# Performance work log

Measured on AMD Instinct MI355X. Metric: run time of the kernel, lower is better.

## Reference

```python
import jax, jax.numpy as jnp
import numpy as np
import math

HID = 128
NH = 8
HD = HID // NH
NL = 3
CLIP = 10.0
EPS = 1e-5

def _ln(x, g, b):
    mu = jnp.mean(x, axis=-1, keepdims=True)
    var = jnp.var(x, axis=-1, keepdims=True)
    return (x - mu) * jax.lax.rsqrt(var + EPS) * g + b

def _layer(h, e_bias1, e_gate2, g1, b1, wh, g2, b2, w1, w2):
    B, N, _ = h.shape
    h_in = h
    hn = _ln(h, g1, b1)
    qkv = hn @ wh                                   # (B,N,3H)
    q, k, v = jnp.split(qkv, 3, axis=-1)
    q = q.reshape(B, N, NH, HD).transpose(0, 2, 1, 3)  # (B,nh,N,hd)
    k = k.reshape(B, N, NH, HD).transpose(0, 2, 1, 3)
    v = v.reshape(B, N, NH, HD).transpose(0, 2, 1, 3)
    att = jnp.einsum('bhid,bhjd->bhij', q, k) * (1.0 / math.sqrt(HD))
    att = jax.nn.softmax(att + e_bias1, axis=-1) * e_gate2
    y = jnp.einsum('bhij,bhjd->bhid', att, v)
    y = y.transpose(0, 2, 1, 3).reshape(B, N, HID)
    z = _ln(y + h_in, g2, b2)
    mlp = jax.nn.relu(z @ w1) @ w2
    return mlp + y

def setup_inputs() -> dict:
    key = jax.random.key(0)
    ks = jax.random.split(key, 9)
    d = {
        'node_features': jax.random.normal(ks[0], (16, 256, 2), jnp.float32),
        'edge_features': jax.random.normal(ks[1], (16, 256, 256, 1), jnp.float32),
        'Wn': jax.random.normal(ks[2], (2, HID), jnp.float32) * 0.5,
        'We_in': jax.random.normal(ks[3], (1, HID), jnp.float32) * 0.1,
        'ln1_g': jnp.ones((NL, HID), jnp.float32),
        'ln1_b': jnp.zeros((NL, HID), jnp.float32),
        'Wh': jax.random.normal(ks[4], (NL, HID, 3 * HID), jnp.float32) * (1.0 / math.sqrt(HID)),
        'We': jax.random.normal(ks[5], (NL, HID, 2 * NH), jnp.float32) * (1.0 / math.sqrt(HID)),
        'ln2_g': jnp.ones((NL, HID), jnp.float32),
        'ln2_b': jnp.zeros((NL, HID), jnp.float32),
        'W1': jax.random.normal(ks[6], (NL, HID, 4 * HID), jnp.float32) * (1.0 / math.sqrt(HID)),
        'W2': jax.random.normal(ks[7], (NL, 4 * HID, HID), jnp.float32) * (1.0 / math.sqrt(4 * HID)),
        'Wdec': jax.random.normal(ks[8], (HID, 1), jnp.float32) * (1.0 / math.sqrt(HID)),
    }
    return d

def reference(node_features, edge_features, Wn, We_in, ln1_g, ln1_b, Wh, We, ln2_g, ln2_b, W1, W2, Wdec):
    h = node_features @ Wn                              # (B,N,H)
    e = edge_features @ We_in                           # (B,N,N,H)
    for i in range(NL):
        ee = e @ We[i]                                  # (B,N,N,2*nh)
        ee = ee.transpose(0, 3, 1, 2)                   # (B,2*nh,N,N)
        e1, e2 = ee[:, :NH], ee[:, NH:]
        h = _layer(h, e1, e2, ln1_g[i], ln1_b[i], Wh[i], ln2_g[i], ln2_b[i], W1[i], W2[i])
    out = h @ Wdec                                      # (B,N,1)
    out = CLIP * jnp.tanh(out / math.sqrt(HID))
    return out
```

## Files before the change

### kernel.cpp

```cpp
#include <hip/hip_runtime.h>
#include <math.h>

#define HID 128
#define NHEAD 8
#define NL 3
#define NS 256
#define ROWS 4096

typedef __attribute__((ext_vector_type(8))) short bf16x8;
typedef __attribute__((ext_vector_type(4))) float f32x4;

__device__ __forceinline__ float us2f(unsigned short s) { return __uint_as_float(((unsigned)s) << 16); }
__device__ __forceinline__ unsigned short f2b(float f) {
    unsigned u = __float_as_uint(f);
    return (unsigned short)((u + 0x7fff + ((u >> 16) & 1)) >> 16);
}

__global__ __launch_bounds__(256) void k_prep(
    const float* __restrict__ Wh, const float* __restrict__ W1, const float* __restrict__ W2,
    const float* __restrict__ We_in, const float* __restrict__ We,
    const float* __restrict__ nf, const float* __restrict__ Wn,
    unsigned short* __restrict__ WhH, unsigned short* __restrict__ WhL,
    unsigned short* __restrict__ W1H, unsigned short* __restrict__ W1L,
    unsigned short* __restrict__ W2H, unsigned short* __restrict__ W2L,
    float* __restrict__ sbuf, float* __restrict__ h)
{
    int b = blockIdx.x, t = threadIdx.x;
    if (b >= 529) {
        int idx = (b - 529) * 256 + t;
        int r = idx >> 7, c = idx & 127;
        h[idx] = nf[2 * r] * Wn[c] + nf[2 * r + 1] * Wn[HID + c];
        return;
    }
    if (b == 528) {
        if (t < NL * 2 * NHEAD) {
            int l = t / (2 * NHEAD), j = t % (2 * NHEAD);
            float acc = 0.f;
            for (int c = 0; c < HID; ++c)
                acc += We_in[c] * We[(long)(l * HID + c) * (2 * NHEAD) + j];
            sbuf[t] = acc;
        }
        return;
    }
    const float* S; unsigned short *OH, *OL; int K, N, kt, nt;
    if (b < 144) {
        int l = b / 48, rem = b % 48; kt = rem & 3; nt = rem >> 2; K = 128; N = 384;
        S = Wh + (long)l * 128 * 384; OH = WhH + (long)l * 384 * 128; OL = WhL + (long)l * 384 * 128;
    } else if (b < 336) {
        int b2 = b - 144; int l = b2 / 64, rem = b2 % 64; kt = rem & 3; nt = rem >> 2; K = 128; N = 512;
        S = W1 + (long)l * 128 * 512; OH = W1H + (long)l * 512 * 128; OL = W1L + (long)l * 512 * 128;
    } else {
        int b2 = b - 336; int l = b2 / 64, rem = b2 % 64; kt = rem & 15; nt = rem >> 4; K = 512; N = 128;
        S = W2 + (long)l * 512 * 128; OH = W2H + (long)l * 128 * 512; OL = W2L + (long)l * 128 * 512;
    }
    __shared__ float sm[32][33];
    int i0 = t >> 5, j = t & 31;
#pragma unroll
    for (int p = 0; p < 4; ++p) {
        int i = i0 + p * 8;
        sm[i][j] = S[(long)(kt * 32 + i) * N + nt * 32 + j];
    }
    __syncthreads();
#pragma unroll
    for (int p = 0; p < 4; ++p) {
        int n = i0 + p * 8;
        float v = sm[j][n];
        unsigned short hh = f2b(v);
        long o = (long)(nt * 32 + n) * K + kt * 32 + j;
        OH[o] = hh; OL[o] = f2b(v - us2f(hh));
    }
}

__global__ __launch_bounds__(256) void k_fgemm(
    const float* __restrict__ x, const float* __restrict__ x2,
    const float* __restrict__ g, const float* __restrict__ b,
    const unsigned short* __restrict__ WH, const unsigned short* __restrict__ WL,
    unsigned short* __restrict__ Ch, unsigned short* __restrict__ Cl,
    int Nc, int mode)
{
    __shared__ unsigned short sAh[64 * 136], sAl[64 * 136];
    __shared__ unsigned short sWh[64 * 136], sWl[64 * 136];
    int t = threadIdx.x;
    int row0 = blockIdx.y * 64, col0 = blockIdx.x * 64;

#pragma unroll
    for (int p = 0; p < 4; ++p) {
        int rr = (t >> 4) + p * 16, ck = t & 15;
        *(uint4*)&sWh[rr * 136 + ck * 8] = *(const uint4*)&WH[(long)(col0 + rr) * 128 + ck * 8];
        *(uint4*)&sWl[rr * 136 + ck * 8] = *(const uint4*)&WL[(long)(col0 + rr) * 128 + ck * 8];
    }
#pragma unroll
    for (int pass = 0; pass < 2; ++pass) {
        int row = pass * 32 + (t >> 3);
        int p = t & 7, cb = p * 16;
        float v[16];
        const float* xp = x + (long)(row0 + row) * HID + cb;
#pragma unroll
        for (int j = 0; j < 16; j += 4) *(float4*)&v[j] = *(const float4*)(xp + j);
        if (x2) {
            const float* yp = x2 + (long)(row0 + row) * HID + cb;
#pragma unroll
            for (int j = 0; j < 16; j += 4) {
                float4 r4 = *(const float4*)(yp + j);
                v[j] += r4.x; v[j+1] += r4.y; v[j+2] += r4.z; v[j+3] += r4.w;
            }
        }
        float s = 0.f, s2 = 0.f;
#pragma unroll
        for (int j = 0; j < 16; ++j) { s += v[j]; s2 += v[j] * v[j]; }
        s  += __shfl_xor(s, 1);  s  += __shfl_xor(s, 2);  s  += __shfl_xor(s, 4);
        s2 += __shfl_xor(s2, 1); s2 += __shfl_xor(s2, 2); s2 += __shfl_xor(s2, 4);
        float mu  = s * (1.f / HID);
        float var = s2 * (1.f / HID) - mu * mu;
        float inv = rsqrtf(var + 1e-5f);
        unsigned short hi[16], lo[16];
#pragma unroll
        for (int j = 0; j < 16; ++j) {
            int c = cb + j;
            float o = (v[j] - mu) * inv * g[c] + b[c];
            hi[j] = f2b(o); lo[j] = f2b(o - us2f(hi[j]));
        }
        *(uint4*)&sAh[row * 136 + cb]     = *(uint4*)&hi[0];
        *(uint4*)&sAh[row * 136 + cb + 8] = *(uint4*)&hi[8];
        *(uint4*)&sAl[row * 136 + cb]     = *(uint4*)&lo[0];
        *(uint4*)&sAl[row * 136 + cb + 8] = *(uint4*)&lo[8];
    }
    __syncthreads();

    int w = t >> 6, lane = t & 63;
    int m = lane & 15, quad = lane >> 4;
    f32x4 acc[4];
#pragma unroll
    for (int i = 0; i < 4; ++i) acc[i] = (f32x4){0.f, 0.f, 0.f, 0.f};
#pragma unroll
    for (int c = 0; c < 4; ++c) {
        bf16x8 ah = *(const bf16x8*)&sAh[(w * 16 + m) * 136 + c * 32 + quad * 8];
        bf16x8 al = *(const bf16x8*)&sAl[(w * 16 + m) * 136 + c * 32 + quad * 8];
#pragma unroll
        for (int nt = 0; nt < 4; ++nt) {
            bf16x8 wh = *(const bf16x8*)&sWh[(nt * 16 + m) * 136 + c * 32 + quad * 8];
            bf16x8 wl = *(const bf16x8*)&sWl[(nt * 16 + m) * 136 + c * 32 + quad * 8];
            acc[nt] = __builtin_amdgcn_mfma_f32_16x16x32_bf16(ah, wh, acc[nt], 0, 0, 0);
            acc[nt] = __builtin_amdgcn_mfma_f32_16x16x32_bf16(ah, wl, acc[nt], 0, 0, 0);
            acc[nt] = __builtin_amdgcn_mfma_f32_16x16x32_bf16(al, wh, acc[nt], 0, 0, 0);
        }
    }
#pragma unroll
    for (int nt = 0; nt < 4; ++nt) {
#pragma unroll
        for (int r = 0; r < 4; ++r) {
            int row = row0 + w * 16 + quad * 4 + r;
            int col = col0 + nt * 16 + m;
            float v = acc[nt][r];
            if (mode) v = fmaxf(v, 0.f);
            unsigned short hh = f2b(v);
            Ch[(long)row * Nc + col] = hh;
            Cl[(long)row * Nc + col] = f2b(v - us2f(hh));
        }
    }
}

__global__ __launch_bounds__(256, 3) void k_w2ln(
    const unsigned short* __restrict__ Ah, const unsigned short* __restrict__ Al,
    const unsigned short* __restrict__ WH, const unsigned short* __restrict__ WL,
    const float* __restrict__ yres, float* __restrict__ hout,
    const float* __restrict__ Wdec, float* __restrict__ out)
{
    __shared__ unsigned short sA[2][16 * 72];
    __shared__ unsigned short sW[2][128 * 72];
    int t = threadIdx.x;
    int row0 = blockIdx.x * 16;
    int w = t >> 6, lane = t & 63;
    int m = lane & 15, quad = lane >> 4;
    f32x4 acc[2];
    acc[0] = (f32x4){0.f,0.f,0.f,0.f}; acc[1] = (f32x4){0.f,0.f,0.f,0.f};

    for (int ks = 0; ks < 512; ks += 64) {
        if (ks) __syncthreads();
        {
            int pl = t >> 7, tt = t & 127;
            int r = tt >> 3, ck = tt & 7;
            const unsigned short* src = pl ? Al : Ah;
            *(uint4*)&sA[pl][r * 72 + ck * 8] = *(const uint4*)&src[(long)(row0 + r) * 512 + ks + ck * 8];
        }
        {
            int r0 = t >> 3, ck = t & 7;
#pragma unroll
            for (int p = 0; p < 4; ++p) {
                int n = r0 + p * 32;
                *(uint4*)&sW[0][n * 72 + ck * 8] = *(const uint4*)&WH[(long)n * 512 + ks + ck * 8];
                *(uint4*)&sW[1][n * 72 + ck * 8] = *(const uint4*)&WL[(long)n * 512 + ks + ck * 8];
            }
        }
        __syncthreads();
#pragma unroll
        for (int c = 0; c < 2; ++c) {
            bf16x8 ah = *(const bf16x8*)&sA[0][m * 72 + c * 32 + quad * 8];
            bf16x8 al = *(const bf16x8*)&sA[1][m * 72 + c * 32 + quad * 8];
#pragma unroll
            for (int nt = 0; nt < 2; ++nt) {
                int n = w * 32 + nt * 16 + m;
                bf16x8 wh = *(const bf16x8*)&sW[0][n * 72 + c * 32 + quad * 8];
                bf16x8 wl = *(const bf16x8*)&sW[1][n * 72 + c * 32 + quad * 8];
                acc[nt] = __builtin_amdgcn_mfma_f32_16x16x32_bf16(ah, wh, acc[nt], 0, 0, 0);
                acc[nt] = __builtin_amdgcn_mfma_f32_16x16x32_bf16(ah, wl, acc[nt], 0, 0, 0);
                acc[nt] = __builtin_amdgcn_mfma_f32_16x16x32_bf16(al, wh, acc[nt], 0, 0, 0);
            }
        }
    }
    __syncthreads();
    float* ht = (float*)&sW[0][0];
#pragma unroll
    for (int nt = 0; nt < 2; ++nt) {
#pragma unroll
        for (int r = 0; r < 4; ++r) {
            int row = quad * 4 + r;
            int col = w * 32 + nt * 16 + m;
            float v = acc[nt][r] + yres[(long)(row0 + row) * HID + col];
            hout[(long)(row0 + row) * HID + col] = v;
            ht[row * 132 + col] = v;
        }
    }
    __syncthreads();
    if (Wdec) {
        int row = t >> 4, sub = t & 15;
        float v[8];
        *(float4*)&v[0] = *(const float4*)&ht[row * 132 + sub * 8];
        *(float4*)&v[4] = *(const float4*)&ht[row * 132 + sub * 8 + 4];
        float a = 0.f;
#pragma unroll
        for (int j = 0; j < 8; ++j) a += v[j] * Wdec[sub * 8 + j];
        a += __shfl_xor(a, 1); a += __shfl_xor(a, 2); a += __shfl_xor(a, 4); a += __shfl_xor(a, 8);
        if (sub == 0) out[row0 + row] = 10.f * tanhf(a * 0.08838834764831845f);
    }
}

#define PAS 268
#define KQS 20
__global__ __launch_bounds__(256) void k_attn(
    const unsigned short* __restrict__ qkvH, const unsigned short* __restrict__ qkvL,
    const float* __restrict__ ef, const float* __restrict__ sbuf,
    int layer, float* __restrict__ y)
{
    __shared__ unsigned short Kh[NS * KQS], Kl[NS * KQS];
    __shared__ unsigned short Qh[64 * KQS], Ql[64 * KQS];
    __shared__ unsigned short Vh[16 * PAS], Vl[16 * PAS];
    __shared__ unsigned short Pa[4][16 * PAS];
    int bid = blockIdx.x;
    int q4 = bid & 3, hh = (bid >> 2) & 7, bb = bid >> 5;
    int t = threadIdx.x;
    {
        long kb = ((long)(bb * NS + t)) * 384 + HID + hh * 16;
        union { uint4 u[2]; unsigned short s[16]; } KH, KL, VH, VL;
        KH.u[0] = *(const uint4*)&qkvH[kb];       KH.u[1] = *(const uint4*)&qkvH[kb + 8];
        KL.u[0] = *(const uint4*)&qkvL[kb];       KL.u[1] = *(const uint4*)&qkvL[kb + 8];
        VH.u[0] = *(const uint4*)&qkvH[kb + 128]; VH.u[1] = *(const uint4*)&qkvH[kb + 136];
        VL.u[0] = *(const uint4*)&qkvL[kb + 128]; VL.u[1] = *(const uint4*)&qkvL[kb + 136];
#pragma unroll
        for (int d = 0; d < 16; ++d) {
            Kh[t * KQS + d] = KH.s[d];
            Kl[t * KQS + d] = KL.s[d];
            Vh[d * PAS + t] = VH.s[d];
            Vl[d * PAS + t] = VL.s[d];
        }
    }
    {
        int row = t >> 2, c4 = (t & 3) * 4;
        long qb = ((long)(bb * NS + q4 * 64 + row)) * 384 + hh * 16 + c4;
        union { uint2 u; unsigned short s[4]; } QH, QL;
        QH.u = *(const uint2*)&qkvH[qb];
        QL.u = *(const uint2*)&qkvL[qb];
#pragma unroll
        for (int j = 0; j < 4; ++j) {
            Qh[row * KQS + c4 + j] = QH.s[j];
            Ql[row * KQS + c4 + j] = QL.s[j];
        }
    }
    __syncthreads();
    int w = t >> 6, lane = t & 63;
    int m = lane & 15, quad = lane >> 4;
    float s1  = sbuf[layer * 16 + hh];
    float s2g = sbuf[layer * 16 + NHEAD + hh];
    unsigned short* Paw = Pa[w];

    bf16x8 qh = (bf16x8){0,0,0,0,0,0,0,0}, ql = qh;
    if (quad < 2) {
        qh = *(const bf16x8*)&Qh[(w * 16 + m) * KQS + quad * 8];
        ql = *(const bf16x8*)&Ql[(w * 16 + m) * KQS + quad * 8];
    }
    f32x4 sc[16];
#pragma unroll
    for (int ct = 0; ct < 16; ++ct) {
        bf16x8 kh = (bf16x8){0,0,0,0,0,0,0,0}, kl = kh;
        if (quad < 2) {
            kh = *(const bf16x8*)&Kh[(ct * 16 + m) * KQS + quad * 8];
            kl = *(const bf16x8*)&Kl[(ct * 16 + m) * KQS + quad * 8];
        }
        f32x4 a = (f32x4){0.f, 0.f, 0.f, 0.f};
        a = __builtin_amdgcn_mfma_f32_16x16x32_bf16(qh, kh, a, 0, 0, 0);
        a = __builtin_amdgcn_mfma_f32_16x16x32_bf16(qh, kl, a, 0, 0, 0);
        a = __builtin_amdgcn_mfma_f32_16x16x32_bf16(ql, kh, a, 0, 0, 0);
        sc[ct] = a;
    }
    int baserow = q4 * 64 + w * 16 + quad * 4;
    float s[4] = {0.f, 0.f, 0.f, 0.f};
#pragma unroll
    for (int ct = 0; ct < 16; ++ct) {
#pragma unroll
        for (int r = 0; r < 4; ++r) {
            float e = ef[((long)(bb * NS + baserow + r)) * NS + ct * 16 + m];
            float p = __expf(sc[ct][r] * 0.25f + e * s1);
            s[r] += p;
            Paw[(quad * 4 + r) * PAS + ct * 16 + m] = f2b(p * e);
        }
    }
    float inv[4];
#pragma unroll
    for (int r = 0; r < 4; ++r) {
        float ss = s[r];
        ss += __shfl_xor(ss, 1); ss += __shfl_xor(ss, 2);
        ss += __shfl_xor(ss, 4); ss += __shfl_xor(ss, 8);
        inv[r] = s2g / ss;
    }
    __syncthreads();
    f32x4 acc = (f32x4){0.f, 0.f, 0.f, 0.f};
#pragma unroll
    for (int sft = 0; sft < 8; ++sft) {
        bf16x8 pf = *(const bf16x8*)&Paw[m * PAS + sft * 32 + quad * 8];
        bf16x8 vh = *(const bf16x8*)&Vh[m * PAS + sft * 32 + quad * 8];
        bf16x8 vl = *(const bf16x8*)&Vl[m * PAS + sft * 32 + quad * 8];
        acc = __builtin_amdgcn_mfma_f32_16x16x32_bf16(pf, vh, acc, 0, 0, 0);
        acc = __builtin_amdgcn_mfma_f32_16x16x32_bf16(pf, vl, acc, 0, 0, 0);
    }
#pragma unroll
    for (int r = 0; r < 4; ++r) {
        int row = q4 * 64 + w * 16 + quad * 4 + r;
        y[((long)(bb * NS + row)) * HID + hh * 16 + m] = acc[r] * inv[r];
    }
}

extern "C" void kernel_launch(void* const* d_in, const int* in_sizes, int n_in,
                              void* d_out, int out_size, void* d_ws, size_t ws_size,
                              hipStream_t stream) {
    const float* nf    = (const float*)d_in[0];
    const float* ef    = (const float*)d_in[1];
    const float* Wn    = (const float*)d_in[2];
    const float* We_in = (const float*)d_in[3];
    const float* ln1g  = (const float*)d_in[4];
    const float* ln1b  = (const float*)d_in[5];
    const float* Wh    = (const float*)d_in[6];
    const float* We    = (const float*)d_in[7];
    const float* ln2g  = (const float*)d_in[8];
    const float* ln2b  = (const float*)d_in[9];
    const float* W1    = (const float*)d_in[10];
    const float* W2    = (const float*)d_in[11];
    const float* Wdec  = (const float*)d_in[12];

    float* ws   = (float*)d_ws;
    float* sbuf = ws;
    float* h    = ws + 64;
    float* y    = h + ROWS * HID;
    unsigned short* qkvH = (unsigned short*)(y + ROWS * HID);
    unsigned short* qkvL = qkvH + (long)ROWS * 384;
    unsigned short* hidH = qkvL + (long)ROWS * 384;
    unsigned short* hidL = hidH + (long)ROWS * 512;
    unsigned short* WhH  = hidL + (long)ROWS * 512;
    unsigned short* WhL  = WhH + (long)NL * 384 * 128;
    unsigned short* W1H  = WhL + (long)NL * 384 * 128;
    unsigned short* W1L  = W1H + (long)NL * 512 * 128;
    unsigned short* W2H  = W1L + (long)NL * 512 * 128;
    unsigned short* W2L  = W2H + (long)NL * 128 * 512;

    k_prep<<<529 + ROWS * HID / 256, 256, 0, stream>>>(Wh, W1, W2, We_in, We, nf, Wn,
                                    WhH, WhL, W1H, W1L, W2H, W2L, sbuf, h);
    for (int l = 0; l < NL; ++l) {
        k_fgemm<<<dim3(6, 64), 256, 0, stream>>>(h, nullptr,
            ln1g + l * HID, ln1b + l * HID,
            WhH + (long)l * 384 * 128, WhL + (long)l * 384 * 128,
            qkvH, qkvL, 384, 0);
        k_attn<<<512, 256, 0, stream>>>(qkvH, qkvL, ef, sbuf, l, y);
        k_fgemm<<<dim3(8, 64), 256, 0, stream>>>(y, h,
            ln2g + l * HID, ln2b + l * HID,
            W1H + (long)l * 512 * 128, W1L + (long)l * 512 * 128,
            hidH, hidL, 512, 1);
        int last = (l == NL - 1);
        k_w2ln<<<ROWS / 16, 256, 0, stream>>>(hidH, hidL,
            W2H + (long)l * 128 * 512, W2L + (long)l * 128 * 512,
            y, h, last ? Wdec : nullptr, (float*)d_out);
    }
}
```

Before: 215.5 us.

## Fuse LN2, W1 GEMM, ReLU and W2 GEMM into one MLP kernel

Replaces the separate LN2+W1 GEMM kernel and the W2 GEMM kernel with one kernel per 16-row tile. The tile does the layernorm, the hi/lo bf16 split, the W1 MFMA and ReLU, keeps the 512-wide hidden activation in shared memory, then runs the W2 MFMA and the residual. This removes the global round trip of the hidden activations and one launch per layer. Weights are now read straight from global memory without LDS staging, and each block has a larger register footprint.

```diff
diff --git a/kernel.cpp b/kernel.cpp
--- a/kernel.cpp
+++ b/kernel.cpp
@@ -160,76 +160,127 @@
     }
 }
 
-__global__ __launch_bounds__(256, 3) void k_w2ln(
-    const unsigned short* __restrict__ Ah, const unsigned short* __restrict__ Al,
-    const unsigned short* __restrict__ WH, const unsigned short* __restrict__ WL,
-    const float* __restrict__ yres, float* __restrict__ hout,
-    const float* __restrict__ Wdec, float* __restrict__ out)
+__global__ __launch_bounds__(256, 1) void k_mlp(
+    const float* __restrict__ y, const float* __restrict__ h,
+    const float* __restrict__ g, const float* __restrict__ b,
+    const unsigned short* __restrict__ W1H_, const unsigned short* __restrict__ W1L_,
+    const unsigned short* __restrict__ W2H_, const unsigned short* __restrict__ W2L_,
+    float* __restrict__ hout, const float* __restrict__ Wdec, float* __restrict__ out)
 {
-    __shared__ unsigned short sA[2][16 * 72];
-    __shared__ unsigned short sW[2][128 * 72];
+    __shared__ __align__(16) unsigned short sAh[16 * 136], sAl[16 * 136];
+    __shared__ __align__(16) unsigned short sHh[16 * 520], sHl[16 * 520];
     int t = threadIdx.x;
     int row0 = blockIdx.x * 16;
+
+    if (t < 128) {
+        int row = t >> 3, p = t & 7, cb = p * 16;
+        float v[16];
+        const float* xp = y + (long)(row0 + row) * HID + cb;
+        const float* hp = h + (long)(row0 + row) * HID + cb;
+#pragma unroll
+        for (int j = 0; j < 16; j += 4) {
+            float4 a4 = *(const float4*)(xp + j);
+            float4 b4 = *(const float4*)(hp + j);
+            v[j] = a4.x + b4.x; v[j+1] = a4.y + b4.y; v[j+2] = a4.z + b4.z; v[j+3] = a4.w + b4.w;
+        }
+        float s = 0.f, s2 = 0.f;
+#pragma unroll
+        for (int j = 0; j < 16; ++j) { s += v[j]; s2 += v[j] * v[j]; }
+        s  += __shfl_xor(s, 1);  s  += __shfl_xor(s, 2);  s  += __shfl_xor(s, 4);
+        s2 += __shfl_xor(s2, 1); s2 += __shfl_xor(s2, 2); s2 += __shfl_xor(s2, 4);
+        float mu  = s * (1.f / HID);
+        float var = s2 * (1.f / HID) - mu * mu;
+        float inv = rsqrtf(var + 1e-5f);
+        unsigned short hi[16], lo[16];
+#pragma unroll
+        for (int j = 0; j < 16; ++j) {
+            int c = cb + j;
+            float o = (v[j] - mu) * inv * g[c] + b[c];
+            hi[j] = f2b(o); lo[j] = f2b(o - us2f(hi[j]));
+        }
+        *(uint4*)&sAh[row * 136 + cb]     = *(uint4*)&hi[0];
+        *(uint4*)&sAh[row * 136 + cb + 8] = *(uint4*)&hi[8];
+        *(uint4*)&sAl[row * 136 + cb]     = *(uint4*)&lo[0];
+        *(uint4*)&sAl[row * 136 + cb + 8] = *(uint4*)&lo[8];
+    }
+    __syncthreads();
+
     int w = t >> 6, lane = t & 63;
     int m = lane & 15, quad = lane >> 4;
-    f32x4 acc[2];
-    acc[0] = (f32x4){0.f,0.f,0.f,0.f}; acc[1] = (f32x4){0.f,0.f,0.f,0.f};
-
-    for (int ks = 0; ks < 512; ks += 64) {
-        if (ks) __syncthreads();
-        {
-            int pl = t >> 7, tt = t & 127;
-            int r = tt >> 3, ck = tt & 7;
-            const unsigned short* src = pl ? Al : Ah;
-            *(uint4*)&sA[pl][r * 72 + ck * 8] = *(const uint4*)&src[(long)(row0 + r) * 512 + ks + ck * 8];
-        }
-        {
-            int r0 = t >> 3, ck = t & 7;
-#pragma unroll
-            for (int p = 0; p < 4; ++p) {
-                int n = r0 + p * 32;
-                *(uint4*)&sW[0][n * 72 + ck * 8] = *(const uint4*)&WH[(long)n * 512 + ks + ck * 8];
-                *(uint4*)&sW[1][n * 72 + ck * 8] = *(const uint4*)&WL[(long)n * 512 + ks + ck * 8];
-            }
-        }
-        __syncthreads();
-#pragma unroll
-        for (int c = 0; c < 2; ++c) {
-            bf16x8 ah = *(const bf16x8*)&sA[0][m * 72 + c * 32 + quad * 8];
-            bf16x8 al = *(const bf16x8*)&sA[1][m * 72 + c * 32 + quad * 8];
-#pragma unroll
-            for (int nt = 0; nt < 2; ++nt) {
-                int n = w * 32 + nt * 16 + m;
-                bf16x8 wh = *(const bf16x8*)&sW[0][n * 72 + c * 32 + quad * 8];
-                bf16x8 wl = *(const bf16x8*)&sW[1][n * 72 + c * 32 + quad * 8];
-                acc[nt] = __builtin_amdgcn_mfma_f32_16x16x32_bf16(ah, wh, acc[nt], 0, 0, 0);
-                acc[nt] = __builtin_amdgcn_mfma_f32_16x16x32_bf16(ah, wl, acc[nt], 0, 0, 0);
-                acc[nt] = __builtin_amdgcn_mfma_f32_16x16x32_bf16(al, wh, acc[nt], 0, 0, 0);
-            }
-        }
-    }
-    __syncthreads();
-    float* ht = (float*)&sW[0][0];
+
+    f32x4 acc1[8];
+#pragma unroll
+    for (int i = 0; i < 8; ++i) acc1[i] = (f32x4){0.f, 0.f, 0.f, 0.f};
+    const unsigned short* w1h = W1H_ + (long)(w * 128 + m) * 128 + quad * 8;
+    const unsigned short* w1l = W1L_ + (long)(w * 128 + m) * 128 + quad * 8;
+#pragma unroll
+    for (int c = 0; c < 4; ++c) {
+        bf16x8 ah = *(const bf16x8*)&sAh[m * 136 + c * 32 + quad * 8];
+        bf16x8 al = *(const bf16x8*)&sAl[m * 136 + c * 32 + quad * 8];
+#pragma unroll
+        for (int nt = 0; nt < 8; ++nt) {
+            bf16x8 wh = *(const bf16x8*)&w1h[nt * 16 * 128 + c * 32];
+            bf16x8 wl = *(const bf16x8*)&w1l[nt * 16 * 128 + c * 32];
+            acc1[nt] = __builtin_amdgcn_mfma_f32_16x16x32_bf16(wh, ah, acc1[nt], 0, 0, 0);
+            acc1[nt] = __builtin_amdgcn_mfma_f32_16x16x32_bf16(wh, al, acc1[nt], 0, 0, 0);
+            acc1[nt] = __builtin_amdgcn_mfma_f32_16x16x32_bf16(wl, ah, acc1[nt], 0, 0, 0);
+        }
+    }
+#pragma unroll
+    for (int nt = 0; nt < 8; ++nt) {
+        unsigned short hi4[4], lo4[4];
+#pragma unroll
+        for (int r = 0; r < 4; ++r) {
+            float v = fmaxf(acc1[nt][r], 0.f);
+            hi4[r] = f2b(v);
+            lo4[r] = f2b(v - us2f(hi4[r]));
+        }
+        int kk = w * 128 + nt * 16 + quad * 4;
+        *(uint2*)&sHh[m * 520 + kk] = *(const uint2*)hi4;
+        *(uint2*)&sHl[m * 520 + kk] = *(const uint2*)lo4;
+    }
+    __syncthreads();
+
+    f32x4 acc2[2];
+    acc2[0] = (f32x4){0.f, 0.f, 0.f, 0.f};
+    acc2[1] = (f32x4){0.f, 0.f, 0.f, 0.f};
+    const unsigned short* w2h = W2H_ + (long)(w * 32 + m) * 512 + quad * 8;
+    const unsigned short* w2l = W2L_ + (long)(w * 32 + m) * 512 + quad * 8;
+#pragma unroll
+    for (int c = 0; c < 16; ++c) {
+        bf16x8 ah = *(const bf16x8*)&sHh[m * 520 + c * 32 + quad * 8];
+        bf16x8 al = *(const bf16x8*)&sHl[m * 520 + c * 32 + quad * 8];
+#pragma unroll
+        for (int nt = 0; nt < 2; ++nt) {
+            bf16x8 wh = *(const bf16x8*)&w2h[nt * 16 * 512 + c * 32];
+            bf16x8 wl = *(const bf16x8*)&w2l[nt * 16 * 512 + c * 32];
+            acc2[nt] = __builtin_amdgcn_mfma_f32_16x16x32_bf16(ah, wh, acc2[nt], 0, 0, 0);
+            acc2[nt] = __builtin_amdgcn_mfma_f32_16x16x32_bf16(ah, wl, acc2[nt], 0, 0, 0);
+            acc2[nt] = __builtin_amdgcn_mfma_f32_16x16x32_bf16(al, wh, acc2[nt], 0, 0, 0);
+        }
+    }
+    __syncthreads();
+    float* ht = (float*)&sHh[0];
 #pragma unroll
     for (int nt = 0; nt < 2; ++nt) {
 #pragma unroll
         for (int r = 0; r < 4; ++r) {
             int row = quad * 4 + r;
             int col = w * 32 + nt * 16 + m;
-            float v = acc[nt][r] + yres[(long)(row0 + row) * HID + col];
+            float v = acc2[nt][r] + y[(long)(row0 + row) * HID + col];
             hout[(long)(row0 + row) * HID + col] = v;
             ht[row * 132 + col] = v;
         }
     }
-    __syncthreads();
     if (Wdec) {
+        __syncthreads();
         int row = t >> 4, sub = t & 15;
-        float v[8];
-        *(float4*)&v[0] = *(const float4*)&ht[row * 132 + sub * 8];
-        *(float4*)&v[4] = *(const float4*)&ht[row * 132 + sub * 8 + 4];
+        float vv[8];
+        *(float4*)&vv[0] = *(const float4*)&ht[row * 132 + sub * 8];
+        *(float4*)&vv[4] = *(const float4*)&ht[row * 132 + sub * 8 + 4];
         float a = 0.f;
 #pragma unroll
-        for (int j = 0; j < 8; ++j) a += v[j] * Wdec[sub * 8 + j];
+        for (int j = 0; j < 8; ++j) a += vv[j] * Wdec[sub * 8 + j];
         a += __shfl_xor(a, 1); a += __shfl_xor(a, 2); a += __shfl_xor(a, 4); a += __shfl_xor(a, 8);
         if (sub == 0) out[row0 + row] = 10.f * tanhf(a * 0.08838834764831845f);
     }
@@ -362,9 +413,7 @@
     float* y    = h + ROWS * HID;
     unsigned short* qkvH = (unsigned short*)(y + ROWS * HID);
     unsigned short* qkvL = qkvH + (long)ROWS * 384;
-    unsigned short* hidH = qkvL + (long)ROWS * 384;
-    unsigned short* hidL = hidH + (long)ROWS * 512;
-    unsigned short* WhH  = hidL + (long)ROWS * 512;
+    unsigned short* WhH  = qkvL + (long)ROWS * 384;
     unsigned short* WhL  = WhH + (long)NL * 384 * 128;
     unsigned short* W1H  = WhL + (long)NL * 384 * 128;
     unsigned short* W1L  = W1H + (long)NL * 512 * 128;
@@ -379,13 +428,11 @@
             WhH + (long)l * 384 * 128, WhL + (long)l * 384 * 128,
             qkvH, qkvL, 384, 0);
         k_attn<<<512, 256, 0, stream>>>(qkvH, qkvL, ef, sbuf, l, y);
-        k_fgemm<<<dim3(8, 64), 256, 0, stream>>>(y, h,
+        int last = (l == NL - 1);
+        k_mlp<<<ROWS / 16, 256, 0, stream>>>(y, h,
             ln2g + l * HID, ln2b + l * HID,
             W1H + (long)l * 512 * 128, W1L + (long)l * 512 * 128,
-            hidH, hidL, 512, 1);
-        int last = (l == NL - 1);
-        k_w2ln<<<ROWS / 16, 256, 0, stream>>>(hidH, hidL,
             W2H + (long)l * 128 * 512, W2L + (long)l * 128 * 512,
-            y, h, last ? Wdec : nullptr, (float*)d_out);
-    }
-}
+            h, last ? Wdec : nullptr, (float*)d_out);
+    }
+}
```

Result: no change. 213.7 us (-0.8%).
